# Kernel tuning notes

Measured on AMD Instinct MI355X. Metric: run time of the kernel, lower is better.

Reference implementation:

```python
import jax, jax.numpy as jnp
import numpy as np

N_NODES = 50000
N_EDGES = 800000
HIDDEN = 64


def _init_linear(key, fan_in, fan_out):
    kw, kb = jax.random.split(key)
    lim = 1.0 / np.sqrt(fan_in)
    W = jax.random.uniform(kw, (fan_in, fan_out), jnp.float32, -lim, lim)
    b = jax.random.uniform(kb, (fan_out,), jnp.float32, -lim, lim)
    return W, b


def setup_inputs() -> dict:
    key = jax.random.key(0)
    ks = jax.random.split(key, 10)
    feat = jax.random.normal(ks[0], (N_NODES, HIDDEN), jnp.float32)
    x = jax.random.normal(ks[1], (N_NODES, 3), jnp.float32)
    src = jax.random.randint(ks[2], (N_EDGES,), 0, N_NODES, jnp.int32)
    dst = jax.random.randint(ks[3], (N_EDGES,), 0, N_NODES, jnp.int32)
    # message MLP: (2H+1) -> H -> H, relu after both layers (last_activation=mid)
    W1, b1 = _init_linear(ks[4], 2 * HIDDEN + 1, HIDDEN)
    W2, b2 = _init_linear(ks[5], HIDDEN, HIDDEN)
    # soft edge gate: H -> 1
    we, be = _init_linear(ks[6], HIDDEN, 1)
    # update MLP: H -> H -> H, relu mid, no last activation
    U1, c1 = _init_linear(ks[7], HIDDEN, HIDDEN)
    U2, c2 = _init_linear(ks[8], HIDDEN, HIDDEN)
    return dict(feat=feat, x=x, src=src, dst=dst,
                W1=W1, b1=b1, W2=W2, b2=b2, we=we, be=be,
                U1=U1, c1=c1, U2=U2, c2=c2)


def reference(feat, x, src, dst, W1, b1, W2, b2, we, be, U1, c1, U2, c2):
    # per-edge squared distance between endpoint coordinates: [E, 1]
    sqd = jnp.sum((x[src] - x[dst]) ** 2, axis=-1, keepdims=True)
    # message input: [E, 2H+1]
    msg_in = jnp.concatenate([feat[src], feat[dst], sqd], axis=-1)
    # 2-layer message MLP with relu mid and last activation
    m = jax.nn.relu(jax.nn.relu(msg_in @ W1 + b1) @ W2 + b2)
    # sigmoid soft-edge gate: [E, 1]
    gate = jax.nn.sigmoid(m @ we + be)
    # scatter-sum gated messages to destination nodes: [N, H]
    m_sum = jax.ops.segment_sum(m * gate, dst, num_segments=N_NODES)
    # node update MLP on (m_sum + feat), residual add
    h = m_sum + feat
    h_new = jax.nn.relu(h @ U1 + c1) @ U2 + c2
    return h_new + feat
```

## Files before the change

### kernel.cpp

```cpp
#include <hip/hip_runtime.h>
#include <hip/hip_bf16.h>
#include <stdint.h>

#define N_NODES 50000
#define N_EDGES 800000
#define HDIM 64
#define SCAN_N (N_NODES + 1)
#define NTILE  3125

#define ESRC_OFF  0
#define ESQD_OFF  3200000
#define DEG_OFF   6400000
#define OFFS_OFF  6604800
#define POS_OFF   6809600
#define FB_OFF    7014400
#define W1T_OFF   13414400
#define W2T_OFF   13430784
#define U1T_OFF   13438976
#define U2T_OFF   13447168
#define WS_NEED   13455360

#define CVT_BLOCKS  1563
#define PREPW_BLOCKS 80
#define HIST_BLOCKS 1024

typedef __attribute__((ext_vector_type(8))) short short8;
typedef __attribute__((ext_vector_type(4))) float floatx4;

__device__ __forceinline__ float bf2f(unsigned short u) {
    union { unsigned int i; float f; } v; v.i = ((unsigned int)u) << 16; return v.f;
}
__device__ __forceinline__ unsigned short f2bf(float f) {
    __hip_bfloat16 h = __float2bfloat16(f);
    return *reinterpret_cast<unsigned short*>(&h);
}

__device__ __forceinline__ int detect_is_bf16(const unsigned short* p) {
    int cnt = 0;
    #pragma unroll
    for (int i = 0; i < 64; ++i) {
        unsigned short b = p[i];
        int e = (b >> 7) & 0xFF;
        cnt += ((e >= 97 && e <= 157) || (b & 0x7FFF) == 0) ? 1 : 0;
    }
    return cnt >= 56;
}

__device__ __forceinline__ float getf(const void* p, unsigned int i, int isb) {
    return isb ? bf2f(((const unsigned short*)p)[i]) : ((const float*)p)[i];
}

__device__ __forceinline__ short8 get8bf(const void* p, unsigned int i, int isb) {
    if (isb) {
        return *reinterpret_cast<const short8*>((const short*)p + i);
    } else {
        const float4 f0 = *reinterpret_cast<const float4*>((const float*)p + i);
        const float4 f1 = *reinterpret_cast<const float4*>((const float*)p + i + 4);
        short8 a;
        a[0] = (short)f2bf(f0.x); a[1] = (short)f2bf(f0.y);
        a[2] = (short)f2bf(f0.z); a[3] = (short)f2bf(f0.w);
        a[4] = (short)f2bf(f1.x); a[5] = (short)f2bf(f1.y);
        a[6] = (short)f2bf(f1.z); a[7] = (short)f2bf(f1.w);
        return a;
    }
}

#define COMPILER_FENCE() asm volatile("" ::: "memory")
#define WAIT_LDS() __builtin_amdgcn_s_waitcnt(0xC07F)

__global__ __launch_bounds__(256) void prep_kernel(
    const void* __restrict__ feat, unsigned short* __restrict__ fb,
    const void* __restrict__ W1, const void* __restrict__ W2,
    const void* __restrict__ U1, const void* __restrict__ U2,
    unsigned short* __restrict__ w1t, unsigned short* __restrict__ w2t,
    unsigned short* __restrict__ u1t, unsigned short* __restrict__ u2t,
    const int* __restrict__ dst, int* __restrict__ deg)
{
    const int b = blockIdx.x;
    if (b < CVT_BLOCKS) {
        const int isb = detect_is_bf16((const unsigned short*)feat);
        int i = (b * 256 + threadIdx.x) * 8;
        if (i >= N_NODES * HDIM) return;
        if (isb) {
            *reinterpret_cast<uint4*>(fb + i) =
                *reinterpret_cast<const uint4*>((const unsigned short*)feat + i);
        } else {
            float4 f0 = *reinterpret_cast<const float4*>((const float*)feat + i);
            float4 f1 = *reinterpret_cast<const float4*>((const float*)feat + i + 4);
            ushort4 a = {f2bf(f0.x), f2bf(f0.y), f2bf(f0.z), f2bf(f0.w)};
            ushort4 c = {f2bf(f1.x), f2bf(f1.y), f2bf(f1.z), f2bf(f1.w)};
            *reinterpret_cast<ushort4*>(fb + i)     = a;
            *reinterpret_cast<ushort4*>(fb + i + 4) = c;
        }
    } else if (b < CVT_BLOCKS + PREPW_BLOCKS) {
        const int isb = detect_is_bf16((const unsigned short*)feat);
        int idx = (b - CVT_BLOCKS) * 256 + threadIdx.x;
        if (idx < 8192) {
            int n = idx >> 7, k = idx & 127;
            w1t[idx] = f2bf(getf(W1, k * 64 + n, isb));
        } else if (idx < 12288) {
            int i = idx - 8192, n = i >> 6, k = i & 63;
            w2t[i] = f2bf(getf(W2, k * 64 + n, isb));
        } else if (idx < 16384) {
            int i = idx - 12288, n = i >> 6, k = i & 63;
            u1t[i] = f2bf(getf(U1, k * 64 + n, isb));
        } else if (idx < 20480) {
            int i = idx - 16384, n = i >> 6, k = i & 63;
            u2t[i] = f2bf(getf(U2, k * 64 + n, isb));
        }
    } else {
        int e0 = (b - CVT_BLOCKS - PREPW_BLOCKS) * 256 + threadIdx.x;
        for (int e = e0; e < N_EDGES; e += HIST_BLOCKS * 256)
            atomicAdd(&deg[dst[e]], 1);
    }
}

__global__ void scan1_kernel(const int* __restrict__ deg, int* __restrict__ part) {
    __shared__ int s[1024];
    int g = blockIdx.x * 1024 + threadIdx.x;
    s[threadIdx.x] = (g < SCAN_N) ? deg[g] : 0;
    __syncthreads();
    for (int off = 512; off > 0; off >>= 1) {
        if (threadIdx.x < off) s[threadIdx.x] += s[threadIdx.x + off];
        __syncthreads();
    }
    if (threadIdx.x == 0) part[blockIdx.x] = s[0];
}

__global__ void scan2_kernel(int* __restrict__ part, int nparts) {
    if (threadIdx.x == 0) {
        int run = 0;
        for (int i = 0; i < nparts; ++i) { int t = part[i]; part[i] = run; run += t; }
    }
}

__global__ void scan3_kernel(const int* __restrict__ deg, const int* __restrict__ part,
                             int* __restrict__ offs, int* __restrict__ pos) {
    __shared__ int s[1024];
    int g = blockIdx.x * 1024 + threadIdx.x;
    int v = (g < SCAN_N) ? deg[g] : 0;
    s[threadIdx.x] = v;
    __syncthreads();
    for (int off = 1; off < 1024; off <<= 1) {
        int t = (threadIdx.x >= off) ? s[threadIdx.x - off] : 0;
        __syncthreads();
        s[threadIdx.x] += t;
        __syncthreads();
    }
    int excl = s[threadIdx.x] - v + part[blockIdx.x];
    if (g < SCAN_N) { offs[g] = excl; pos[g] = excl; }
}

__global__ __launch_bounds__(256) void fill_kernel(
    const int* __restrict__ src, const int* __restrict__ dst,
    const void* __restrict__ xpos, const void* __restrict__ feat,
    int* __restrict__ pos, int* __restrict__ esrc, float* __restrict__ esqd)
{
    const int isb = detect_is_bf16((const unsigned short*)feat);
    for (int e = blockIdx.x * 256 + threadIdx.x; e < N_EDGES; e += gridDim.x * 256) {
        int s = src[e], d = dst[e];
        int slot = atomicAdd(&pos[d], 1);
        float dx = getf(xpos, s * 3 + 0, isb) - getf(xpos, d * 3 + 0, isb);
        float dy = getf(xpos, s * 3 + 1, isb) - getf(xpos, d * 3 + 1, isb);
        float dz = getf(xpos, s * 3 + 2, isb) - getf(xpos, d * 3 + 2, isb);
        esrc[slot] = s;
        esqd[slot] = dx * dx + dy * dy + dz * dz;
    }
}

__global__ __launch_bounds__(256, 2) void fused_kernel(
    const unsigned short* __restrict__ fbf,
    const unsigned short* __restrict__ w1t, const unsigned short* __restrict__ w2t,
    const unsigned short* __restrict__ u1t, const unsigned short* __restrict__ u2t,
    const int* __restrict__ esrc, const float* __restrict__ esqd,
    const int* __restrict__ offs,
    const void* __restrict__ feat,
    const void* __restrict__ W1, const void* __restrict__ b1,
    const void* __restrict__ b2, const void* __restrict__ we,
    const void* __restrict__ be,
    const void* __restrict__ c1v, const void* __restrict__ c2v,
    void* __restrict__ out)
{
    __shared__ __align__(16) short sW1[16][64][8];
    __shared__ __align__(16) short sW2[8][64][8];
    __shared__ __align__(16) short sA2[4][16][72];
    __shared__ __align__(16) float sH[4][16][68];

    const int isb  = detect_is_bf16((const unsigned short*)feat);
    const int tid  = threadIdx.x;
    const int wave = tid >> 6;
    const int lane = tid & 63;
    const int l15  = lane & 15;
    const int quad = lane >> 4;
    const int rowb = quad * 4;

    for (int i = tid; i < 16 * 64; i += 256) {
        int f = i >> 6, l = i & 63;
        int n = (f & 3) * 16 + (l & 15);
        int k0 = (f >> 2) * 32 + (l >> 4) * 8;
        *reinterpret_cast<short8*>(&sW1[f][l][0]) =
            *reinterpret_cast<const short8*>(w1t + n * 128 + k0);
    }
    for (int i = tid; i < 8 * 64; i += 256) {
        int f = i >> 6, l = i & 63;
        int n = (f & 3) * 16 + (l & 15);
        int k0 = (f >> 2) * 32 + (l >> 4) * 8;
        *reinterpret_cast<short8*>(&sW2[f][l][0]) =
            *reinterpret_cast<const short8*>(w2t + n * 64 + k0);
    }
    __syncthreads();

    float b1r[4], w1lr[4], b2r[4], wer[4];
    #pragma unroll
    for (int nt = 0; nt < 4; ++nt) {
        int n = nt * 16 + l15;
        b1r[nt]  = getf(b1, n, isb);
        w1lr[nt] = getf(W1, 128 * 64 + n, isb);
        b2r[nt]  = getf(b2, n, isb);
        wer[nt]  = getf(we, n, isb);
    }
    const float ber = getf(be, 0, isb);

    const int t = blockIdx.x * 4 + wave;
    if (t < NTILE) {
        const int nb = t * 16;

        int off_l = 0;
        if (lane < 17) off_l = offs[nb + lane];

        for (int nl = 0; nl < 16; ++nl) {
            const int s  = __shfl(off_l, nl);
            const int en = __shfl(off_l, nl + 1);
            const int dn = nb + nl;
            const short8 ad0 = *reinterpret_cast<const short8*>(fbf + dn * 64 + quad * 8);
            const short8 ad1 = *reinterpret_cast<const short8*>(fbf + dn * 64 + 32 + quad * 8);

            float macc[4] = {0.f, 0.f, 0.f, 0.f};

            for (int cb = s; cb < en; cb += 16) {
                const int rem = en - cb;
                const int myr = (l15 < rem) ? l15 : (rem - 1);
                const int sn      = esrc[cb + myr];
                const float sqd_l = esqd[cb + myr];

                floatx4 acc[4];
                #pragma unroll
                for (int nt = 0; nt < 4; ++nt) acc[nt] = (floatx4){0.f, 0.f, 0.f, 0.f};
                #pragma unroll
                for (int c = 0; c < 4; ++c) {
                    short8 a;
                    if (c == 0)      a = *reinterpret_cast<const short8*>(fbf + sn * 64 + quad * 8);
                    else if (c == 1) a = *reinterpret_cast<const short8*>(fbf + sn * 64 + 32 + quad * 8);
                    else if (c == 2) a = ad0;
                    else             a = ad1;
                    #pragma unroll
                    for (int nt = 0; nt < 4; ++nt) {
                        short8 b = *reinterpret_cast<const short8*>(&sW1[c * 4 + nt][lane][0]);
                        acc[nt] = __builtin_amdgcn_mfma_f32_16x16x32_bf16(a, b, acc[nt], 0, 0, 0);
                    }
                }

                float sq[4];
                #pragma unroll
                for (int r = 0; r < 4; ++r) sq[r] = __shfl(sqd_l, rowb + r);
                #pragma unroll
                for (int nt = 0; nt < 4; ++nt)
                    #pragma unroll
                    for (int r = 0; r < 4; ++r) {
                        float v = fmaxf(acc[nt][r] + b1r[nt] + sq[r] * w1lr[nt], 0.f);
                        sA2[wave][rowb + r][nt * 16 + l15] = (short)f2bf(v);
                    }
                COMPILER_FENCE();
                WAIT_LDS();

                floatx4 acc2[4];
                #pragma unroll
                for (int nt = 0; nt < 4; ++nt) acc2[nt] = (floatx4){0.f, 0.f, 0.f, 0.f};
                #pragma unroll
                for (int c = 0; c < 2; ++c) {
                    short8 a = *reinterpret_cast<const short8*>(&sA2[wave][l15][c * 32 + quad * 8]);
                    #pragma unroll
                    for (int nt = 0; nt < 4; ++nt) {
                        short8 b = *reinterpret_cast<const short8*>(&sW2[c * 4 + nt][lane][0]);
                        acc2[nt] = __builtin_amdgcn_mfma_f32_16x16x32_bf16(a, b, acc2[nt], 0, 0, 0);
                    }
                }
                COMPILER_FENCE();

                float mval[4][4];
                float part[4] = {0.f, 0.f, 0.f, 0.f};
                #pragma unroll
                for (int nt = 0; nt < 4; ++nt)
                    #pragma unroll
                    for (int r = 0; r < 4; ++r) {
                        float v = fmaxf(acc2[nt][r] + b2r[nt], 0.f);
                        mval[nt][r] = v;
                        part[r] += v * wer[nt];
                    }
                #pragma unroll
                for (int off = 1; off < 16; off <<= 1)
                    #pragma unroll
                    for (int r = 0; r < 4; ++r) part[r] += __shfl_xor(part[r], off);

                float gacc[4] = {0.f, 0.f, 0.f, 0.f};
                #pragma unroll
                for (int r = 0; r < 4; ++r) {
                    int row = rowb + r;
                    float g = (row < rem) ? 1.f / (1.f + __expf(-(part[r] + ber))) : 0.f;
                    #pragma unroll
                    for (int nt = 0; nt < 4; ++nt) gacc[nt] += mval[nt][r] * g;
                }
                #pragma unroll
                for (int nt = 0; nt < 4; ++nt) {
                    float p = gacc[nt];
                    p += __shfl_xor(p, 16);
                    p += __shfl_xor(p, 32);
                    macc[nt] += p;
                }
            }

            if (quad == 0) {
                #pragma unroll
                for (int nt = 0; nt < 4; ++nt)
                    sH[wave][nl][nt * 16 + l15] = macc[nt];
            }
        }
        COMPILER_FENCE();
        WAIT_LDS();

        short8 u1f[2][4], u2f[2][4];
        #pragma unroll
        for (int nt = 0; nt < 4; ++nt) {
            const int n = nt * 16 + l15;
            #pragma unroll
            for (int c = 0; c < 2; ++c) {
                u1f[c][nt] = *reinterpret_cast<const short8*>(u1t + n * 64 + c * 32 + quad * 8);
                u2f[c][nt] = *reinterpret_cast<const short8*>(u2t + n * 64 + c * 32 + quad * 8);
            }
        }
        float c1r[4], c2r[4];
        #pragma unroll
        for (int nt = 0; nt < 4; ++nt) {
            c1r[nt] = getf(c1v, nt * 16 + l15, isb);
            c2r[nt] = getf(c2v, nt * 16 + l15, isb);
        }

        const int node = nb + l15;

        short8 ah[2];
        #pragma unroll
        for (int c = 0; c < 2; ++c) {
            float4 m0 = *reinterpret_cast<const float4*>(&sH[wave][l15][c * 32 + quad * 8]);
            float4 m1 = *reinterpret_cast<const float4*>(&sH[wave][l15][c * 32 + quad * 8 + 4]);
            float ms[8] = {m0.x, m0.y, m0.z, m0.w, m1.x, m1.y, m1.z, m1.w};
            unsigned int off = (unsigned int)node * 64u + c * 32 + quad * 8;
            float hv[8];
            if (isb) {
                short8 fv = *reinterpret_cast<const short8*>((const short*)feat + off);
                #pragma unroll
                for (int j = 0; j < 8; ++j) hv[j] = bf2f((unsigned short)fv[j]);
            } else {
                float4 f0 = *reinterpret_cast<const float4*>((const float*)feat + off);
                float4 f1 = *reinterpret_cast<const float4*>((const float*)feat + off + 4);
                hv[0] = f0.x; hv[1] = f0.y; hv[2] = f0.z; hv[3] = f0.w;
                hv[4] = f1.x; hv[5] = f1.y; hv[6] = f1.z; hv[7] = f1.w;
            }
            short8 a;
            #pragma unroll
            for (int j = 0; j < 8; ++j) a[j] = (short)f2bf(ms[j] + hv[j]);
            ah[c] = a;
        }

        floatx4 acc[4];
        #pragma unroll
        for (int nt = 0; nt < 4; ++nt) acc[nt] = (floatx4){0.f, 0.f, 0.f, 0.f};
        #pragma unroll
        for (int c = 0; c < 2; ++c)
            #pragma unroll
            for (int nt = 0; nt < 4; ++nt)
                acc[nt] = __builtin_amdgcn_mfma_f32_16x16x32_bf16(ah[c], u1f[c][nt], acc[nt], 0, 0, 0);
        #pragma unroll
        for (int nt = 0; nt < 4; ++nt)
            #pragma unroll
            for (int r = 0; r < 4; ++r) {
                float v = fmaxf(acc[nt][r] + c1r[nt], 0.f);
                sA2[wave][rowb + r][nt * 16 + l15] = (short)f2bf(v);
            }
        COMPILER_FENCE();
        WAIT_LDS();

        floatx4 acc2[4];
        #pragma unroll
        for (int nt = 0; nt < 4; ++nt) acc2[nt] = (floatx4){0.f, 0.f, 0.f, 0.f};
        #pragma unroll
        for (int c = 0; c < 2; ++c) {
            short8 a = *reinterpret_cast<const short8*>(&sA2[wave][l15][c * 32 + quad * 8]);
            #pragma unroll
            for (int nt = 0; nt < 4; ++nt)
                acc2[nt] = __builtin_amdgcn_mfma_f32_16x16x32_bf16(a, u2f[c][nt], acc2[nt], 0, 0, 0);
        }
        COMPILER_FENCE();

        #pragma unroll
        for (int nt = 0; nt < 4; ++nt)
            #pragma unroll
            for (int r = 0; r < 4; ++r)
                sH[wave][rowb + r][nt * 16 + l15] = acc2[nt][r] + c2r[nt];
        COMPILER_FENCE();
        WAIT_LDS();

        const unsigned int ob = (unsigned int)node * 64u + quad * 16;
        if (isb) {
            const unsigned short* fp = (const unsigned short*)feat + ob;
            unsigned short* op = (unsigned short*)out + ob;
            #pragma unroll
            for (int k = 0; k < 2; ++k) {
                ushort4 o0, o1;
                float4 v0 = *reinterpret_cast<const float4*>(&sH[wave][l15][quad * 16 + k * 8]);
                float4 v1 = *reinterpret_cast<const float4*>(&sH[wave][l15][quad * 16 + k * 8 + 4]);
                const ushort4 f0 = *reinterpret_cast<const ushort4*>(fp + k * 8);
                const ushort4 f1 = *reinterpret_cast<const ushort4*>(fp + k * 8 + 4);
                o0.x = f2bf(v0.x + bf2f(f0.x)); o0.y = f2bf(v0.y + bf2f(f0.y));
                o0.z = f2bf(v0.z + bf2f(f0.z)); o0.w = f2bf(v0.w + bf2f(f0.w));
                o1.x = f2bf(v1.x + bf2f(f1.x)); o1.y = f2bf(v1.y + bf2f(f1.y));
                o1.z = f2bf(v1.z + bf2f(f1.z)); o1.w = f2bf(v1.w + bf2f(f1.w));
                *reinterpret_cast<ushort4*>(op + k * 8)     = o0;
                *reinterpret_cast<ushort4*>(op + k * 8 + 4) = o1;
            }
        } else {
            const float* fp = (const float*)feat + ob;
            float* op = (float*)out + ob;
            #pragma unroll
            for (int k = 0; k < 4; ++k) {
                float4 v = *reinterpret_cast<const float4*>(&sH[wave][l15][quad * 16 + k * 4]);
                float4 f = *reinterpret_cast<const float4*>(fp + k * 4);
                float4 o = {v.x + f.x, v.y + f.y, v.z + f.z, v.w + f.w};
                *reinterpret_cast<float4*>(op + k * 4) = o;
            }
        }
    }
}

__global__ __launch_bounds__(256, 2) void edge_kernel_atomic(
    const void* __restrict__ feat, const void* __restrict__ xpos,
    const int* __restrict__ src, const int* __restrict__ dst,
    const void* __restrict__ W1, const void* __restrict__ b1,
    const void* __restrict__ W2, const void* __restrict__ b2,
    const void* __restrict__ we, const void* __restrict__ be,
    float* __restrict__ msum, unsigned int msum_cap)
{
    __shared__ __align__(16) short sA2[4][16][72];

    const int isb  = detect_is_bf16((const unsigned short*)feat);
    const int tid  = threadIdx.x;
    const int wave = tid >> 6;
    const int lane = tid & 63;
    const int l15  = lane & 15;
    const int quad = lane >> 4;

    short8 bw1[4][4], bw2[2][4];
    #pragma unroll
    for (int c = 0; c < 4; ++c)
        #pragma unroll
        for (int nt = 0; nt < 4; ++nt) {
            short8 b;
            #pragma unroll
            for (int j = 0; j < 8; ++j)
                b[j] = (short)f2bf(getf(W1, (c * 32 + quad * 8 + j) * 64 + nt * 16 + l15, isb));
            bw1[c][nt] = b;
        }
    #pragma unroll
    for (int c = 0; c < 2; ++c)
        #pragma unroll
        for (int nt = 0; nt < 4; ++nt) {
            short8 b;
            #pragma unroll
            for (int j = 0; j < 8; ++j)
                b[j] = (short)f2bf(getf(W2, (c * 32 + quad * 8 + j) * 64 + nt * 16 + l15, isb));
            bw2[c][nt] = b;
        }
    float b1r[4], w1lr[4], b2r[4], wer[4];
    #pragma unroll
    for (int nt = 0; nt < 4; ++nt) {
        int n = nt * 16 + l15;
        b1r[nt]  = getf(b1, n, isb);
        w1lr[nt] = getf(W1, 128 * 64 + n, isb);
        b2r[nt]  = getf(b2, n, isb);
        wer[nt]  = getf(we, n, isb);
    }
    const float ber = getf(be, 0, isb);
    const int rowb = quad * 4;

    const int ntiles = N_EDGES / 64;
    for (int t = blockIdx.x; t < ntiles; t += gridDim.x) {
        const int ebase = t * 64 + wave * 16;
        int sidx = 0, didx = 0;
        float sqd = 0.f;
        if (lane < 16) {
            int e = ebase + lane;
            sidx = src[e]; didx = dst[e];
            float dx = getf(xpos, sidx * 3 + 0, isb) - getf(xpos, didx * 3 + 0, isb);
            float dy = getf(xpos, sidx * 3 + 1, isb) - getf(xpos, didx * 3 + 1, isb);
            float dz = getf(xpos, sidx * 3 + 2, isb) - getf(xpos, didx * 3 + 2, isb);
            sqd = dx * dx + dy * dy + dz * dz;
        }
        const int sn = __shfl(sidx, l15);
        const int dn_row = __shfl(didx, l15);

        floatx4 acc[4];
        #pragma unroll
        for (int nt = 0; nt < 4; ++nt) acc[nt] = (floatx4){0.f, 0.f, 0.f, 0.f};
        #pragma unroll
        for (int c = 0; c < 4; ++c) {
            const int node = (c < 2) ? sn : dn_row;
            short8 a = get8bf(feat, (unsigned int)node * 64u + (c & 1) * 32 + quad * 8, isb);
            #pragma unroll
            for (int nt = 0; nt < 4; ++nt)
                acc[nt] = __builtin_amdgcn_mfma_f32_16x16x32_bf16(a, bw1[c][nt], acc[nt], 0, 0, 0);
        }
        float sq[4];
        #pragma unroll
        for (int r = 0; r < 4; ++r) sq[r] = __shfl(sqd, rowb + r);
        #pragma unroll
        for (int nt = 0; nt < 4; ++nt)
            #pragma unroll
            for (int r = 0; r < 4; ++r) {
                float v = fmaxf(acc[nt][r] + b1r[nt] + sq[r] * w1lr[nt], 0.f);
                sA2[wave][rowb + r][nt * 16 + l15] = (short)f2bf(v);
            }
        COMPILER_FENCE();
        WAIT_LDS();
        floatx4 acc2[4];
        #pragma unroll
        for (int nt = 0; nt < 4; ++nt) acc2[nt] = (floatx4){0.f, 0.f, 0.f, 0.f};
        #pragma unroll
        for (int c = 0; c < 2; ++c) {
            short8 a = *reinterpret_cast<const short8*>(&sA2[wave][l15][c * 32 + quad * 8]);
            #pragma unroll
            for (int nt = 0; nt < 4; ++nt)
                acc2[nt] = __builtin_amdgcn_mfma_f32_16x16x32_bf16(a, bw2[c][nt], acc2[nt], 0, 0, 0);
        }
        COMPILER_FENCE();
        float mval[4][4], part[4] = {0.f, 0.f, 0.f, 0.f};
        #pragma unroll
        for (int nt = 0; nt < 4; ++nt)
            #pragma unroll
            for (int r = 0; r < 4; ++r) {
                float v = fmaxf(acc2[nt][r] + b2r[nt], 0.f);
                mval[nt][r] = v;
                part[r] += v * wer[nt];
            }
        #pragma unroll
        for (int off = 1; off < 16; off <<= 1)
            #pragma unroll
            for (int r = 0; r < 4; ++r) part[r] += __shfl_xor(part[r], off);
        #pragma unroll
        for (int r = 0; r < 4; ++r) {
            int dn = __shfl(didx, rowb + r);
            float g = 1.f / (1.f + __expf(-(part[r] + ber)));
            unsigned int base = (unsigned int)dn * 64u;
            if (base + 64u <= msum_cap) {
                #pragma unroll
                for (int nt = 0; nt < 4; ++nt)
                    unsafeAtomicAdd(&msum[base + nt * 16 + l15], mval[nt][r] * g);
            }
        }
    }
}

__global__ __launch_bounds__(256, 2) void node_kernel_atomic(
    const float* __restrict__ msum, const void* __restrict__ feat,
    const void* __restrict__ U1, const void* __restrict__ c1v,
    const void* __restrict__ U2, const void* __restrict__ c2v,
    void* __restrict__ out, unsigned int msum_cap)
{
    __shared__ __align__(16) short sT[4][16][72];

    const int isb  = detect_is_bf16((const unsigned short*)feat);
    const int tid  = threadIdx.x;
    const int wave = tid >> 6;
    const int lane = tid & 63;
    const int l15  = lane & 15;
    const int quad = lane >> 4;

    short8 u1f[2][4], u2f[2][4];
    #pragma unroll
    for (int c = 0; c < 2; ++c)
        #pragma unroll
        for (int nt = 0; nt < 4; ++nt) {
            short8 a, b;
            #pragma unroll
            for (int j = 0; j < 8; ++j) {
                int k = c * 32 + quad * 8 + j, n = nt * 16 + l15;
                a[j] = (short)f2bf(getf(U1, k * 64 + n, isb));
                b[j] = (short)f2bf(getf(U2, k * 64 + n, isb));
            }
            u1f[c][nt] = a; u2f[c][nt] = b;
        }
    float c1r[4], c2r[4];
    #pragma unroll
    for (int nt = 0; nt < 4; ++nt) {
        c1r[nt] = getf(c1v, nt * 16 + l15, isb);
        c2r[nt] = getf(c2v, nt * 16 + l15, isb);
    }
    const int rowb = quad * 4;

    const int t = blockIdx.x * 4 + wave;
    if (t < NTILE) {
        const int node = t * 16 + l15;
        short8 ah[2];
        #pragma unroll
        for (int c = 0; c < 2; ++c) {
            unsigned int off = (unsigned int)node * 64u + c * 32 + quad * 8;
            float hv[8];
            if (isb) {
                short8 fv = *reinterpret_cast<const short8*>((const short*)feat + off);
                #pragma unroll
                for (int j = 0; j < 8; ++j) hv[j] = bf2f((unsigned short)fv[j]);
            } else {
                float4 f0 = *reinterpret_cast<const float4*>((const float*)feat + off);
                float4 f1 = *reinterpret_cast<const float4*>((const float*)feat + off + 4);
                hv[0] = f0.x; hv[1] = f0.y; hv[2] = f0.z; hv[3] = f0.w;
                hv[4] = f1.x; hv[5] = f1.y; hv[6] = f1.z; hv[7] = f1.w;
            }
            float4 m0 = *reinterpret_cast<const float4*>(msum + off);
            float4 m1 = *reinterpret_cast<const float4*>(msum + off + 4);
            hv[0] += m0.x; hv[1] += m0.y; hv[2] += m0.z; hv[3] += m0.w;
            hv[4] += m1.x; hv[5] += m1.y; hv[6] += m1.z; hv[7] += m1.w;
            short8 a;
            #pragma unroll
            for (int j = 0; j < 8; ++j) a[j] = (short)f2bf(hv[j]);
            ah[c] = a;
        }
        floatx4 acc[4];
        #pragma unroll
        for (int nt = 0; nt < 4; ++nt) acc[nt] = (floatx4){0.f, 0.f, 0.f, 0.f};
        #pragma unroll
        for (int c = 0; c < 2; ++c)
            #pragma unroll
            for (int nt = 0; nt < 4; ++nt)
                acc[nt] = __builtin_amdgcn_mfma_f32_16x16x32_bf16(ah[c], u1f[c][nt], acc[nt], 0, 0, 0);
        #pragma unroll
        for (int nt = 0; nt < 4; ++nt)
            #pragma unroll
            for (int r = 0; r < 4; ++r) {
                float v = fmaxf(acc[nt][r] + c1r[nt], 0.f);
                sT[wave][rowb + r][nt * 16 + l15] = (short)f2bf(v);
            }
        COMPILER_FENCE();
        WAIT_LDS();
        floatx4 acc2[4];
        #pragma unroll
        for (int nt = 0; nt < 4; ++nt) acc2[nt] = (floatx4){0.f, 0.f, 0.f, 0.f};
        #pragma unroll
        for (int c = 0; c < 2; ++c) {
            short8 a = *reinterpret_cast<const short8*>(&sT[wave][l15][c * 32 + quad * 8]);
            #pragma unroll
            for (int nt = 0; nt < 4; ++nt)
                acc2[nt] = __builtin_amdgcn_mfma_f32_16x16x32_bf16(a, u2f[c][nt], acc2[nt], 0, 0, 0);
        }
        COMPILER_FENCE();
        #pragma unroll
        for (int r = 0; r < 4; ++r) {
            unsigned int row = (unsigned int)(t * 16 + rowb + r);
            #pragma unroll
            for (int nt = 0; nt < 4; ++nt) {
                unsigned int off = row * 64u + nt * 16 + l15;
                float v = acc2[nt][r] + c2r[nt] + getf(feat, off, isb);
                if (isb) ((unsigned short*)out)[off] = f2bf(v);
                else     ((float*)out)[off] = v;
            }
        }
    }
}

extern "C" void kernel_launch(void* const* d_in, const int* in_sizes, int n_in,
                              void* d_out, int out_size, void* d_ws, size_t ws_size,
                              hipStream_t stream) {
    const void* feat = d_in[0];
    const void* x    = d_in[1];
    const int* src   = (const int*)d_in[2];
    const int* dst   = (const int*)d_in[3];
    const void* W1   = d_in[4];
    const void* b1   = d_in[5];
    const void* W2   = d_in[6];
    const void* b2   = d_in[7];
    const void* we   = d_in[8];
    const void* be   = d_in[9];
    const void* U1   = d_in[10];
    const void* c1   = d_in[11];
    const void* U2   = d_in[12];
    const void* c2   = d_in[13];
    char* ws = (char*)d_ws;

    if (ws_size >= WS_NEED) {
        int* esrc   = (int*)(ws + ESRC_OFF);
        float* esqd = (float*)(ws + ESQD_OFF);
        int* deg    = (int*)(ws + DEG_OFF);
        int* offs   = (int*)(ws + OFFS_OFF);
        int* pos    = (int*)(ws + POS_OFF);
        unsigned short* fb  = (unsigned short*)(ws + FB_OFF);
        unsigned short* w1t = (unsigned short*)(ws + W1T_OFF);
        unsigned short* w2t = (unsigned short*)(ws + W2T_OFF);
        unsigned short* u1t = (unsigned short*)(ws + U1T_OFF);
        unsigned short* u2t = (unsigned short*)(ws + U2T_OFF);

        hipMemsetAsync(deg, 0, 204800, stream);
        prep_kernel<<<CVT_BLOCKS + PREPW_BLOCKS + HIST_BLOCKS, 256, 0, stream>>>(
            feat, fb, W1, W2, U1, U2, w1t, w2t, u1t, u2t, dst, deg);
        scan1_kernel<<<49, 1024, 0, stream>>>(deg, offs + 51200 - 64);
        scan2_kernel<<<1, 64, 0, stream>>>(offs + 51200 - 64, 49);
        scan3_kernel<<<49, 1024, 0, stream>>>(deg, offs + 51200 - 64, offs, pos);
        fill_kernel<<<1024, 256, 0, stream>>>(src, dst, x, feat, pos, esrc, esqd);
        fused_kernel<<<(NTILE + 3) / 4, 256, 0, stream>>>(
            fb, w1t, w2t, u1t, u2t, esrc, esqd, offs, feat,
            W1, b1, b2, we, be, c1, c2, d_out);
    } else {
        float* msum = (float*)ws;
        size_t need = (size_t)N_NODES * HDIM * sizeof(float);
        size_t clr  = need < ws_size ? need : ws_size;
        unsigned int cap = (unsigned int)(ws_size / sizeof(float));
        if (cap > (unsigned int)(N_NODES * HDIM)) cap = (unsigned int)(N_NODES * HDIM);

        hipMemsetAsync(msum, 0, clr, stream);
        edge_kernel_atomic<<<2500, 256, 0, stream>>>(feat, x, src, dst, W1, b1, W2, b2,
                                                     we, be, msum, cap);
        node_kernel_atomic<<<(NTILE + 3) / 4, 256, 0, stream>>>(msum, feat, U1, c1,
                                                                U2, c2, d_out, cap);
    }
}
```

Baseline: 304.0 us.

## Split fused kernel into per-node aggregation and separate node MLP kernel

Replaces the fused kernel, where each wave serially processed 16 destination nodes, with an aggregation kernel assigning one wave per destination node and writing message sums to a global workspace buffer. A separate node kernel then reads those sums and applies the update MLP. This aims to expose far more parallelism and hide gather latency. It costs an extra global round trip for the sums, an extra launch, and much more redundant per-block staging of weights into shared memory.

```diff
diff --git a/kernel.cpp b/kernel.cpp
--- a/kernel.cpp
+++ b/kernel.cpp
@@ -18,7 +18,8 @@
 #define W2T_OFF   13430784
 #define U1T_OFF   13438976
 #define U2T_OFF   13447168
-#define WS_NEED   13455360
+#define MSUM_OFF  13455360
+#define WS_NEED   (MSUM_OFF + (size_t)N_NODES * HDIM * 4)
 
 #define CVT_BLOCKS  1563
 #define PREPW_BLOCKS 80
@@ -168,23 +169,20 @@
     }
 }
 
-__global__ __launch_bounds__(256, 2) void fused_kernel(
+__global__ __launch_bounds__(256, 2) void agg_kernel(
     const unsigned short* __restrict__ fbf,
     const unsigned short* __restrict__ w1t, const unsigned short* __restrict__ w2t,
-    const unsigned short* __restrict__ u1t, const unsigned short* __restrict__ u2t,
     const int* __restrict__ esrc, const float* __restrict__ esqd,
     const int* __restrict__ offs,
     const void* __restrict__ feat,
     const void* __restrict__ W1, const void* __restrict__ b1,
     const void* __restrict__ b2, const void* __restrict__ we,
     const void* __restrict__ be,
-    const void* __restrict__ c1v, const void* __restrict__ c2v,
-    void* __restrict__ out)
+    float* __restrict__ msum)
 {
     __shared__ __align__(16) short sW1[16][64][8];
     __shared__ __align__(16) short sW2[8][64][8];
     __shared__ __align__(16) short sA2[4][16][72];
-    __shared__ __align__(16) float sH[4][16][68];
 
     const int isb  = detect_is_bf16((const unsigned short*)feat);
     const int tid  = threadIdx.x;
@@ -221,139 +219,151 @@
     }
     const float ber = getf(be, 0, isb);
 
+    const int dn = blockIdx.x * 4 + wave;
+    if (dn < N_NODES) {
+        const int s  = offs[dn];
+        const int en = offs[dn + 1];
+        const short8 ad0 = *reinterpret_cast<const short8*>(fbf + dn * 64 + quad * 8);
+        const short8 ad1 = *reinterpret_cast<const short8*>(fbf + dn * 64 + 32 + quad * 8);
+
+        float macc[4] = {0.f, 0.f, 0.f, 0.f};
+
+        for (int cb = s; cb < en; cb += 16) {
+            const int rem = en - cb;
+            const int myr = (l15 < rem) ? l15 : (rem - 1);
+            const int sn      = esrc[cb + myr];
+            const float sqd_l = esqd[cb + myr];
+
+            floatx4 acc[4];
+            #pragma unroll
+            for (int nt = 0; nt < 4; ++nt) acc[nt] = (floatx4){0.f, 0.f, 0.f, 0.f};
+            #pragma unroll
+            for (int c = 0; c < 4; ++c) {
+                short8 a;
+                if (c == 0)      a = *reinterpret_cast<const short8*>(fbf + sn * 64 + quad * 8);
+                else if (c == 1) a = *reinterpret_cast<const short8*>(fbf + sn * 64 + 32 + quad * 8);
+                else if (c == 2) a = ad0;
+                else             a = ad1;
+                #pragma unroll
+                for (int nt = 0; nt < 4; ++nt) {
+                    short8 b = *reinterpret_cast<const short8*>(&sW1[c * 4 + nt][lane][0]);
+                    acc[nt] = __builtin_amdgcn_mfma_f32_16x16x32_bf16(a, b, acc[nt], 0, 0, 0);
+                }
+            }
+
+            float sq[4];
+            #pragma unroll
+            for (int r = 0; r < 4; ++r) sq[r] = __shfl(sqd_l, rowb + r);
+            #pragma unroll
+            for (int nt = 0; nt < 4; ++nt)
+                #pragma unroll
+                for (int r = 0; r < 4; ++r) {
+                    float v = fmaxf(acc[nt][r] + b1r[nt] + sq[r] * w1lr[nt], 0.f);
+                    sA2[wave][rowb + r][nt * 16 + l15] = (short)f2bf(v);
+                }
+            COMPILER_FENCE();
+            WAIT_LDS();
+
+            floatx4 acc2[4];
+            #pragma unroll
+            for (int nt = 0; nt < 4; ++nt) acc2[nt] = (floatx4){0.f, 0.f, 0.f, 0.f};
+            #pragma unroll
+            for (int c = 0; c < 2; ++c) {
+                short8 a = *reinterpret_cast<const short8*>(&sA2[wave][l15][c * 32 + quad * 8]);
+                #pragma unroll
+                for (int nt = 0; nt < 4; ++nt) {
+                    short8 b = *reinterpret_cast<const short8*>(&sW2[c * 4 + nt][lane][0]);
+                    acc2[nt] = __builtin_amdgcn_mfma_f32_16x16x32_bf16(a, b, acc2[nt], 0, 0, 0);
+                }
+            }
+            COMPILER_FENCE();
+
+            float mval[4][4];
+            float part[4] = {0.f, 0.f, 0.f, 0.f};
+            #pragma unroll
+            for (int nt = 0; nt < 4; ++nt)
+                #pragma unroll
+                for (int r = 0; r < 4; ++r) {
+                    float v = fmaxf(acc2[nt][r] + b2r[nt], 0.f);
+                    mval[nt][r] = v;
+                    part[r] += v * wer[nt];
+                }
+            #pragma unroll
+            for (int off = 1; off < 16; off <<= 1)
+                #pragma unroll
+                for (int r = 0; r < 4; ++r) part[r] += __shfl_xor(part[r], off);
+
+            float gacc[4] = {0.f, 0.f, 0.f, 0.f};
+            #pragma unroll
+            for (int r = 0; r < 4; ++r) {
+                int row = rowb + r;
+                float g = (row < rem) ? 1.f / (1.f + __expf(-(part[r] + ber))) : 0.f;
+                #pragma unroll
+                for (int nt = 0; nt < 4; ++nt) gacc[nt] += mval[nt][r] * g;
+            }
+            #pragma unroll
+            for (int nt = 0; nt < 4; ++nt) {
+                float p = gacc[nt];
+                p += __shfl_xor(p, 16);
+                p += __shfl_xor(p, 32);
+                macc[nt] += p;
+            }
+        }
+
+        if (quad == 0) {
+            #pragma unroll
+            for (int nt = 0; nt < 4; ++nt)
+                msum[(size_t)dn * 64 + nt * 16 + l15] = macc[nt];
+        }
+    }
+}
+
+__global__ __launch_bounds__(256, 2) void node_kernel(
+    const float* __restrict__ msum,
+    const unsigned short* __restrict__ u1t, const unsigned short* __restrict__ u2t,
+    const void* __restrict__ feat,
+    const void* __restrict__ c1v, const void* __restrict__ c2v,
+    void* __restrict__ out)
+{
+    __shared__ __align__(16) short sT[4][16][72];
+    __shared__ __align__(16) float sF[4][16][68];
+
+    const int isb  = detect_is_bf16((const unsigned short*)feat);
+    const int tid  = threadIdx.x;
+    const int wave = tid >> 6;
+    const int lane = tid & 63;
+    const int l15  = lane & 15;
+    const int quad = lane >> 4;
+    const int rowb = quad * 4;
+
+    short8 u1f[2][4], u2f[2][4];
+    #pragma unroll
+    for (int nt = 0; nt < 4; ++nt) {
+        const int n = nt * 16 + l15;
+        #pragma unroll
+        for (int c = 0; c < 2; ++c) {
+            u1f[c][nt] = *reinterpret_cast<const short8*>(u1t + n * 64 + c * 32 + quad * 8);
+            u2f[c][nt] = *reinterpret_cast<const short8*>(u2t + n * 64 + c * 32 + quad * 8);
+        }
+    }
+    float c1r[4], c2r[4];
+    #pragma unroll
+    for (int nt = 0; nt < 4; ++nt) {
+        c1r[nt] = getf(c1v, nt * 16 + l15, isb);
+        c2r[nt] = getf(c2v, nt * 16 + l15, isb);
+    }
+
     const int t = blockIdx.x * 4 + wave;
     if (t < NTILE) {
-        const int nb = t * 16;
-
-        int off_l = 0;
-        if (lane < 17) off_l = offs[nb + lane];
-
-        for (int nl = 0; nl < 16; ++nl) {
-            const int s  = __shfl(off_l, nl);
-            const int en = __shfl(off_l, nl + 1);
-            const int dn = nb + nl;
-            const short8 ad0 = *reinterpret_cast<const short8*>(fbf + dn * 64 + quad * 8);
-            const short8 ad1 = *reinterpret_cast<const short8*>(fbf + dn * 64 + 32 + quad * 8);
-
-            float macc[4] = {0.f, 0.f, 0.f, 0.f};
-
-            for (int cb = s; cb < en; cb += 16) {
-                const int rem = en - cb;
-                const int myr = (l15 < rem) ? l15 : (rem - 1);
-                const int sn      = esrc[cb + myr];
-                const float sqd_l = esqd[cb + myr];
-
-                floatx4 acc[4];
-                #pragma unroll
-                for (int nt = 0; nt < 4; ++nt) acc[nt] = (floatx4){0.f, 0.f, 0.f, 0.f};
-                #pragma unroll
-                for (int c = 0; c < 4; ++c) {
-                    short8 a;
-                    if (c == 0)      a = *reinterpret_cast<const short8*>(fbf + sn * 64 + quad * 8);
-                    else if (c == 1) a = *reinterpret_cast<const short8*>(fbf + sn * 64 + 32 + quad * 8);
-                    else if (c == 2) a = ad0;
-                    else             a = ad1;
-                    #pragma unroll
-                    for (int nt = 0; nt < 4; ++nt) {
-                        short8 b = *reinterpret_cast<const short8*>(&sW1[c * 4 + nt][lane][0]);
-                        acc[nt] = __builtin_amdgcn_mfma_f32_16x16x32_bf16(a, b, acc[nt], 0, 0, 0);
-                    }
-                }
-
-                float sq[4];
-                #pragma unroll
-                for (int r = 0; r < 4; ++r) sq[r] = __shfl(sqd_l, rowb + r);
-                #pragma unroll
-                for (int nt = 0; nt < 4; ++nt)
-                    #pragma unroll
-                    for (int r = 0; r < 4; ++r) {
-                        float v = fmaxf(acc[nt][r] + b1r[nt] + sq[r] * w1lr[nt], 0.f);
-                        sA2[wave][rowb + r][nt * 16 + l15] = (short)f2bf(v);
-                    }
-                COMPILER_FENCE();
-                WAIT_LDS();
-
-                floatx4 acc2[4];
-                #pragma unroll
-                for (int nt = 0; nt < 4; ++nt) acc2[nt] = (floatx4){0.f, 0.f, 0.f, 0.f};
-                #pragma unroll
-                for (int c = 0; c < 2; ++c) {
-                    short8 a = *reinterpret_cast<const short8*>(&sA2[wave][l15][c * 32 + quad * 8]);
-                    #pragma unroll
-                    for (int nt = 0; nt < 4; ++nt) {
-                        short8 b = *reinterpret_cast<const short8*>(&sW2[c * 4 + nt][lane][0]);
-                        acc2[nt] = __builtin_amdgcn_mfma_f32_16x16x32_bf16(a, b, acc2[nt], 0, 0, 0);
-                    }
-                }
-                COMPILER_FENCE();
-
-                float mval[4][4];
-                float part[4] = {0.f, 0.f, 0.f, 0.f};
-                #pragma unroll
-                for (int nt = 0; nt < 4; ++nt)
-                    #pragma unroll
-                    for (int r = 0; r < 4; ++r) {
-                        float v = fmaxf(acc2[nt][r] + b2r[nt], 0.f);
-                        mval[nt][r] = v;
-                        part[r] += v * wer[nt];
-                    }
-                #pragma unroll
-                for (int off = 1; off < 16; off <<= 1)
-                    #pragma unroll
-                    for (int r = 0; r < 4; ++r) part[r] += __shfl_xor(part[r], off);
-
-                float gacc[4] = {0.f, 0.f, 0.f, 0.f};
-                #pragma unroll
-                for (int r = 0; r < 4; ++r) {
-                    int row = rowb + r;
-                    float g = (row < rem) ? 1.f / (1.f + __expf(-(part[r] + ber))) : 0.f;
-                    #pragma unroll
-                    for (int nt = 0; nt < 4; ++nt) gacc[nt] += mval[nt][r] * g;
-                }
-                #pragma unroll
-                for (int nt = 0; nt < 4; ++nt) {
-                    float p = gacc[nt];
-                    p += __shfl_xor(p, 16);
-                    p += __shfl_xor(p, 32);
-                    macc[nt] += p;
-                }
-            }
-
-            if (quad == 0) {
-                #pragma unroll
-                for (int nt = 0; nt < 4; ++nt)
-                    sH[wave][nl][nt * 16 + l15] = macc[nt];
-            }
-        }
-        COMPILER_FENCE();
-        WAIT_LDS();
-
-        short8 u1f[2][4], u2f[2][4];
-        #pragma unroll
-        for (int nt = 0; nt < 4; ++nt) {
-            const int n = nt * 16 + l15;
-            #pragma unroll
-            for (int c = 0; c < 2; ++c) {
-                u1f[c][nt] = *reinterpret_cast<const short8*>(u1t + n * 64 + c * 32 + quad * 8);
-                u2f[c][nt] = *reinterpret_cast<const short8*>(u2t + n * 64 + c * 32 + quad * 8);
-            }
-        }
-        float c1r[4], c2r[4];
-        #pragma unroll
-        for (int nt = 0; nt < 4; ++nt) {
-            c1r[nt] = getf(c1v, nt * 16 + l15, isb);
-            c2r[nt] = getf(c2v, nt * 16 + l15, isb);
-        }
-
-        const int node = nb + l15;
+        const int node = t * 16 + l15;
 
         short8 ah[2];
         #pragma unroll
         for (int c = 0; c < 2; ++c) {
-            float4 m0 = *reinterpret_cast<const float4*>(&sH[wave][l15][c * 32 + quad * 8]);
-            float4 m1 = *reinterpret_cast<const float4*>(&sH[wave][l15][c * 32 + quad * 8 + 4]);
+            unsigned int off = (unsigned int)node * 64u + c * 32 + quad * 8;
+            float4 m0 = *reinterpret_cast<const float4*>(msum + off);
+            float4 m1 = *reinterpret_cast<const float4*>(msum + off + 4);
             float ms[8] = {m0.x, m0.y, m0.z, m0.w, m1.x, m1.y, m1.z, m1.w};
-            unsigned int off = (unsigned int)node * 64u + c * 32 + quad * 8;
             float hv[8];
             if (isb) {
                 short8 fv = *reinterpret_cast<const short8*>((const short*)feat + off);
@@ -384,7 +394,7 @@
             #pragma unroll
             for (int r = 0; r < 4; ++r) {
                 float v = fmaxf(acc[nt][r] + c1r[nt], 0.f);
-                sA2[wave][rowb + r][nt * 16 + l15] = (short)f2bf(v);
+                sT[wave][rowb + r][nt * 16 + l15] = (short)f2bf(v);
             }
         COMPILER_FENCE();
         WAIT_LDS();
@@ -394,7 +404,7 @@
         for (int nt = 0; nt < 4; ++nt) acc2[nt] = (floatx4){0.f, 0.f, 0.f, 0.f};
         #pragma unroll
         for (int c = 0; c < 2; ++c) {
-            short8 a = *reinterpret_cast<const short8*>(&sA2[wave][l15][c * 32 + quad * 8]);
+            short8 a = *reinterpret_cast<const short8*>(&sT[wave][l15][c * 32 + quad * 8]);
             #pragma unroll
             for (int nt = 0; nt < 4; ++nt)
                 acc2[nt] = __builtin_amdgcn_mfma_f32_16x16x32_bf16(a, u2f[c][nt], acc2[nt], 0, 0, 0);
@@ -405,7 +415,7 @@
         for (int nt = 0; nt < 4; ++nt)
             #pragma unroll
             for (int r = 0; r < 4; ++r)
-                sH[wave][rowb + r][nt * 16 + l15] = acc2[nt][r] + c2r[nt];
+                sF[wave][rowb + r][nt * 16 + l15] = acc2[nt][r] + c2r[nt];
         COMPILER_FENCE();
         WAIT_LDS();
 
@@ -416,8 +426,8 @@
             #pragma unroll
             for (int k = 0; k < 2; ++k) {
                 ushort4 o0, o1;
-                float4 v0 = *reinterpret_cast<const float4*>(&sH[wave][l15][quad * 16 + k * 8]);
-                float4 v1 = *reinterpret_cast<const float4*>(&sH[wave][l15][quad * 16 + k * 8 + 4]);
+                float4 v0 = *reinterpret_cast<const float4*>(&sF[wave][l15][quad * 16 + k * 8]);
+                float4 v1 = *reinterpret_cast<const float4*>(&sF[wave][l15][quad * 16 + k * 8 + 4]);
                 const ushort4 f0 = *reinterpret_cast<const ushort4*>(fp + k * 8);
                 const ushort4 f1 = *reinterpret_cast<const ushort4*>(fp + k * 8 + 4);
                 o0.x = f2bf(v0.x + bf2f(f0.x)); o0.y = f2bf(v0.y + bf2f(f0.y));
@@ -432,7 +442,7 @@
             float* op = (float*)out + ob;
             #pragma unroll
             for (int k = 0; k < 4; ++k) {
-                float4 v = *reinterpret_cast<const float4*>(&sH[wave][l15][quad * 16 + k * 4]);
+                float4 v = *reinterpret_cast<const float4*>(&sF[wave][l15][quad * 16 + k * 4]);
                 float4 f = *reinterpret_cast<const float4*>(fp + k * 4);
                 float4 o = {v.x + f.x, v.y + f.y, v.z + f.z, v.w + f.w};
                 *reinterpret_cast<float4*>(op + k * 4) = o;
@@ -704,6 +714,7 @@
         unsigned short* w2t = (unsigned short*)(ws + W2T_OFF);
         unsigned short* u1t = (unsigned short*)(ws + U1T_OFF);
         unsigned short* u2t = (unsigned short*)(ws + U2T_OFF);
+        float* msum = (float*)(ws + MSUM_OFF);
 
         hipMemsetAsync(deg, 0, 204800, stream);
         prep_kernel<<<CVT_BLOCKS + PREPW_BLOCKS + HIST_BLOCKS, 256, 0, stream>>>(
@@ -712,9 +723,10 @@
         scan2_kernel<<<1, 64, 0, stream>>>(offs + 51200 - 64, 49);
         scan3_kernel<<<49, 1024, 0, stream>>>(deg, offs + 51200 - 64, offs, pos);
         fill_kernel<<<1024, 256, 0, stream>>>(src, dst, x, feat, pos, esrc, esqd);
-        fused_kernel<<<(NTILE + 3) / 4, 256, 0, stream>>>(
-            fb, w1t, w2t, u1t, u2t, esrc, esqd, offs, feat,
-            W1, b1, b2, we, be, c1, c2, d_out);
+        agg_kernel<<<(N_NODES + 3) / 4, 256, 0, stream>>>(
+            fb, w1t, w2t, esrc, esqd, offs, feat, W1, b1, b2, we, be, msum);
+        node_kernel<<<(NTILE + 3) / 4, 256, 0, stream>>>(
+            msum, u1t, u2t, feat, c1, c2, d_out);
     } else {
         float* msum = (float*)ws;
         size_t need = (size_t)N_NODES * HDIM * sizeof(float);
```

New measurement: 319.2 us. 1.05x slower.
